# Optimization experiments

Hardware: AMD Instinct MI355X
Metric: run time of the kernel (lower is better)

The kernel has to match this reference:

```python
import jax, jax.numpy as jnp
import numpy as np
from jax import lax

B, IN_N, OUT_N, SEQ, HID = 8, 16, 16, 256, 64
NUM_C = 64 + 3  # grid_size + spline_order
EPS_LN = 1e-5


def setup_inputs():
    key = jax.random.key(0)
    k = jax.random.split(key, 8)
    f32 = jnp.float32
    return {
        "x_in": jax.random.normal(k[0], (B, IN_N, SEQ, HID), f32),
        "proj_x_prev": jax.random.normal(k[1], (B, IN_N, SEQ, HID), f32),
        "spline_weights": jax.random.normal(k[2], (IN_N, OUT_N, NUM_C), f32) * 0.1,
        "base_scales": 0.6 + 0.1 * jax.random.normal(k[3], (IN_N, OUT_N), f32),
        "tau": jax.random.normal(k[4], (IN_N, OUT_N), f32) * 0.1 + 0.1,
        "temperature": jnp.array(1.0, f32),
        "omiga": jnp.full((IN_N, OUT_N), 0.2, f32),
        "W2": jax.random.normal(k[5], (OUT_N, HID, HID), f32) / np.sqrt(HID).astype(np.float32),
        "b_param": jnp.zeros((OUT_N, SEQ, HID), f32),
        "ln_w": jnp.ones((OUT_N, HID), f32),
        "ln_b": jnp.zeros((OUT_N, HID), f32),
        "alpha": jnp.full((OUT_N,), 0.5, f32),
        "beta": jnp.ones((OUT_N,), f32),
        "gamma": jnp.full((OUT_N,), 0.5, f32),
        "theta": jnp.ones((OUT_N,), f32),
        "conv_w": jax.random.normal(k[6], (OUT_N, HID, 1, 3, 3), f32) * 0.1,
    }


def _layernorm(x, w=None, b=None):
    mu = jnp.mean(x, -1, keepdims=True)
    var = jnp.mean((x - mu) ** 2, -1, keepdims=True)
    y = (x - mu) / jnp.sqrt(var + EPS_LN)
    if w is not None:
        y = y * w + b
    return y


def _dwconv(x, w):
    # x: [b, C, 16, 16]; w: [C, 1, 3, 3]; depthwise conv, SAME padding
    return lax.conv_general_dilated(
        x, w, (1, 1), "SAME",
        dimension_numbers=("NCHW", "OIHW", "NCHW"),
        feature_group_count=x.shape[1])


def _forward(x_in, proj_x_prev, spline_weights, base_scales, tau, temperature,
             omiga, W2, b_param, ln_w, ln_b, alpha, beta, gamma, theta, conv_w):
    b, in_n, seq, feat = x_in.shape
    num_c = spline_weights.shape[-1]
    grid = jnp.linspace(-1.0, 1.0, num_c)
    h = 2.0 / (num_c - 1)

    x_energy = jnp.mean(x_in, -1)  # [b,i,s]
    x_norm = jnp.clip(
        x_energy / (jnp.max(jnp.abs(x_energy), -1, keepdims=True) + 1e-8),
        -0.99, 0.99)

    # cubic B-spline basis (masked branches -> nested where)
    dist = jnp.abs(x_norm[..., None] - grid) / h  # [b,i,s,c]
    basis = jnp.where(dist < 1.0, 2.0 / 3.0 - dist ** 2 + dist ** 3 / 2.0,
            jnp.where(dist < 2.0, (2.0 - dist) ** 3 / 6.0, jnp.zeros_like(dist)))

    base_feat = jax.nn.silu(x_norm)[:, :, None, :] * base_scales[None, :, :, None]  # [b,i,j,s]
    spline_feat = jnp.einsum("bisc,ijc->bijs", basis, spline_weights)
    edge_resp = base_feat + spline_feat
    # [b,i,j,s,f]
    activated = (edge_resp[..., None] + jnp.abs(omiga)[None, :, :, None, None]) * x_in[:, :, None]

    t_val = jnp.abs(temperature) + 1e-4
    edge_energies = jnp.mean(jnp.abs(activated), axis=(-1, -2))  # [b,i,j]
    tau_abs = jnp.abs(tau)  # [i,j]
    mask = jax.nn.sigmoid((edge_energies - tau_abs[None]) / t_val)  # [b,i,j]

    # attention kernel W1, vectorized over output neuron j
    mid = in_n // 2
    mult = edge_energies / (tau_abs[None] + 1e-8)  # [b,i,j]
    wp = proj_x_prev[:, :, None] * (mult * mask)[..., None, None]  # [b,i,j,s,d]
    d = wp.shape[-1]
    K = jnp.transpose(wp[:, :mid], (0, 2, 3, 1, 4)).reshape(b, -1, seq, mid * d)
    Q = jnp.transpose(wp[:, mid:2 * mid], (0, 2, 3, 1, 4)).reshape(b, -1, seq, mid * d)
    K, Q = _layernorm(K), _layernorm(Q)
    raw = jnp.einsum("bjsk,bjtk->bjst", K, Q) / (jnp.sqrt(jnp.float32(mid * d)) * t_val)
    W1 = jax.nn.softmax(raw, axis=-1)  # [b,j,s,s]

    # masked mean over input neurons -> per-neuron SplineWeightLayer (vectorized)
    x = jnp.mean(activated * mask[..., None, None], axis=1)  # [b,j,s,f]
    xn = _layernorm(x, ln_w[None, :, None, :], ln_b[None, :, None, :])
    x_prime = jnp.einsum("bjsf,jfo->bjso", xn, W2) + b_param[None]  # [b,j,s,o]
    o = x_prime.shape[-1]

    # depthwise 3x3 conv on 16x16 spatial view, per-j kernels
    xsp = jnp.transpose(x_prime, (1, 0, 3, 2)).reshape(-1, b, o, 16, 16)  # [j,b,o,16,16]
    w3 = jax.vmap(_dwconv)(xsp, conv_w)  # [j,b,o,16,16]
    w3 = jnp.transpose(w3.reshape(-1, b, o, seq), (1, 0, 3, 2))  # [b,j,s,o]

    eye = jnp.eye(seq, dtype=x_prime.dtype)
    ak = (jnp.abs(beta)[None, :, None, None] * W1
          + jnp.abs(alpha)[None, :, None, None] * eye[None, None])
    glob = jnp.einsum("bjst,bjto->bjso", ak, x_prime)
    combined = glob + jnp.abs(theta)[None, :, None, None] * w3
    # residual_proj is Identity since in_hidden == out_hidden
    out = combined + gamma[None, :, None, None] * x
    return out, x_prime  # both [b, out_n, seq, out_hidden]


def reference(x_in, proj_x_prev, spline_weights, base_scales, tau, temperature,
              omiga, W2, b_param, ln_w, ln_b, alpha, beta, gamma, theta, conv_w):
    return _forward(x_in, proj_x_prev, spline_weights, base_scales, tau, temperature,
                    omiga, W2, b_param, ln_w, ln_b, alpha, beta, gamma, theta, conv_w)
```

## Files before the change

kernel.cpp:

```cpp
#include <hip/hip_runtime.h>

#define EPSLN 1e-5f

typedef short bf16x8 __attribute__((ext_vector_type(8)));
typedef float f32x4 __attribute__((ext_vector_type(4)));
typedef unsigned short u16;
typedef unsigned short u16x8 __attribute__((ext_vector_type(8)));

__device__ __forceinline__ float wsum(float v){
  #pragma unroll
  for(int o=32;o;o>>=1) v += __shfl_xor(v,o);
  return v;
}
__device__ __forceinline__ float wmax(float v){
  #pragma unroll
  for(int o=32;o;o>>=1) v = fmaxf(v,__shfl_xor(v,o));
  return v;
}
__device__ __forceinline__ u16 f2bf(float f){
  unsigned int u = __float_as_uint(f);
  u = (u + 0x7FFFu + ((u>>16)&1u)) >> 16;
  return (u16)u;
}
__device__ __forceinline__ float bf2f(u16 h){
  return __uint_as_float(((unsigned int)h)<<16);
}

__global__ void __launch_bounds__(256) kA(
                   const float* __restrict__ xin, const float* __restrict__ p,
                   const float* __restrict__ W2,
                   float* __restrict__ xe, float* __restrict__ xa,
                   float* __restrict__ Sv, float* __restrict__ SSv,
                   u16* __restrict__ xinb, u16* __restrict__ phi, u16* __restrict__ plo,
                   u16* __restrict__ w2B){
  int t = threadIdx.x;
  int rl = t>>3, q = t&7;
  int row = blockIdx.x*32 + rl;
  const float4* xr = (const float4*)(xin + row*64 + q*8);
  const float4* pr = (const float4*)(p   + row*64 + q*8);
  float s1=0.f,s2=0.f,s3=0.f,s4=0.f;
  u16x8 xb, ph, pl;
  #pragma unroll
  for(int k=0;k<2;k++){
    float4 xv = xr[k];
    float4 pv = pr[k];
    s1 += xv.x+xv.y+xv.z+xv.w;
    s2 += fabsf(xv.x)+fabsf(xv.y)+fabsf(xv.z)+fabsf(xv.w);
    s3 += pv.x+pv.y+pv.z+pv.w;
    s4 += pv.x*pv.x+pv.y*pv.y+pv.z*pv.z+pv.w*pv.w;
    int o = k*4;
    xb[o+0]=f2bf(xv.x); xb[o+1]=f2bf(xv.y); xb[o+2]=f2bf(xv.z); xb[o+3]=f2bf(xv.w);
    u16 h0=f2bf(pv.x), h1=f2bf(pv.y), h2=f2bf(pv.z), h3=f2bf(pv.w);
    ph[o+0]=h0; ph[o+1]=h1; ph[o+2]=h2; ph[o+3]=h3;
    pl[o+0]=f2bf(pv.x-bf2f(h0)); pl[o+1]=f2bf(pv.y-bf2f(h1));
    pl[o+2]=f2bf(pv.z-bf2f(h2)); pl[o+3]=f2bf(pv.w-bf2f(h3));
  }
  *(u16x8*)(xinb + row*64 + q*8) = xb;
  *(u16x8*)(phi  + row*64 + q*8) = ph;
  *(u16x8*)(plo  + row*64 + q*8) = pl;
  s1 += __shfl_xor(s1,1); s1 += __shfl_xor(s1,2); s1 += __shfl_xor(s1,4);
  s2 += __shfl_xor(s2,1); s2 += __shfl_xor(s2,2); s2 += __shfl_xor(s2,4);
  s3 += __shfl_xor(s3,1); s3 += __shfl_xor(s3,2); s3 += __shfl_xor(s3,4);
  s4 += __shfl_xor(s4,1); s4 += __shfl_xor(s4,2); s4 += __shfl_xor(s4,4);
  if(q==0){ xe[row]=s1*(1.f/64.f); xa[row]=s2*(1.f/64.f); Sv[row]=s3; SSv[row]=s4; }
  if(blockIdx.x<16){
    int j = blockIdx.x;
    for(int idx=threadIdx.x; idx<4096; idx+=256){
      int f = idx>>6, o = idx&63;
      float v = W2[j*4096 + idx];
      int ks = f>>5, kb = (f>>3)&3, i = f&7;
      int nt = o>>4, col = o&15;
      int ln = kb*16 + col;
      w2B[((j*2+ks)*4 + nt)*512 + ln*8 + i] = f2bf(v);
    }
  }
}

__global__ void __launch_bounds__(256) kBE(
                   const float* __restrict__ xe, const float* __restrict__ sw,
                   const float* __restrict__ bs, const float* __restrict__ om,
                   const float* __restrict__ xa, const float* __restrict__ tau,
                   const float* __restrict__ temp,
                   u16* __restrict__ er2b, float* __restrict__ mask,
                   float* __restrict__ cc,
                   const u16* __restrict__ phi, const u16* __restrict__ plo,
                   float* __restrict__ G){
  __shared__ __align__(16) unsigned char shm[32768];
  int tid = threadIdx.x;
  if(blockIdx.x < 128){
    float* swL = (float*)shm;
    float* bsL = swL + 1072;
    float* omL = bsL + 16;
    float* red = omL + 16;
    float* redE= red + 4;
    int bi = blockIdx.x;
    int i = bi & 15;
    int w = tid>>6, lane = tid&63;
    for(int k=tid;k<16*67;k+=256) swL[k] = sw[i*16*67 + k];
    if(tid<16){ bsL[tid]=bs[i*16+tid]; omL[tid]=fabsf(om[i*16+tid]); }
    float v = xe[bi*256+tid];
    float m = wmax(fabsf(v));
    if(lane==0) red[w]=m;
    __syncthreads();
    m = fmaxf(fmaxf(red[0],red[1]),fmaxf(red[2],red[3]));
    float xn = v/(m+1e-8f);
    xn = fminf(fmaxf(xn,-0.99f),0.99f);
    float sil = xn/(1.f+expf(-xn));
    float vv = (xn+1.f)*33.f;
    int c0 = (int)floorf(vv)-1;
    float acc[16];
    #pragma unroll
    for(int j=0;j<16;j++) acc[j]=0.f;
    #pragma unroll
    for(int k=0;k<4;k++){
      int c = c0+k;
      if(c<0||c>66) continue;
      float d = fabsf(vv-(float)c);
      float bas = d<1.f ? (2.f/3.f - d*d + d*d*d*0.5f)
                : (d<2.f ? (2.f-d)*(2.f-d)*(2.f-d)*(1.f/6.f) : 0.f);
      #pragma unroll
      for(int j=0;j<16;j++) acc[j] += bas*swL[j*67+c];
    }
    float xav = xa[bi*256+tid];
    #pragma unroll
    for(int j=0;j<16;j++){
      float ev = sil*bsL[j] + acc[j] + omL[j];
      er2b[(bi*16+j)*256+tid] = f2bf(ev);
      float pe = wsum(fabsf(ev)*xav);
      if(lane==0) redE[j*4+w]=pe;
    }
    __syncthreads();
    if(tid<16){
      float e = (redE[tid*4+0]+redE[tid*4+1]+redE[tid*4+2]+redE[tid*4+3])*(1.f/256.f);
      float tv = fabsf(temp[0])+1e-4f;
      float ta = fabsf(tau[i*16+tid]);
      float mk = 1.f/(1.f+expf(-(e-ta)/tv));
      mask[bi*16+tid]=mk;
      cc[bi*16+tid]= e/(ta+1e-8f)*mk;
    }
  } else {
    u16* AfB = (u16*)shm;
    u16* BfB = AfB + 8192;
    int e = blockIdx.x - 128;
    int b = e&7, m = (e>>3)&7, sx = (e>>6)&3, ty = e>>8;
    int bm = b*8+m;
    int s0 = sx*64, t0 = ty*64;
    int row = tid>>2, dseg = tid&3;
    size_t offA = ((size_t)(b*16+m  )*256 + s0 + row)*64 + dseg*16;
    size_t offB = ((size_t)(b*16+m+8)*256 + t0 + row)*64 + dseg*16;
    int d0 = dseg*16;
    int ks0 = d0>>5, kb0 = (d0>>3)&3;
    int ks1 = (d0+8)>>5, kb1 = ((d0+8)>>3)&3;
    int lr = row&15, stile = row>>4;
    #define AOFF(h,stl,ks,ln) (((((h)*4+(stl))*2+(ks))*64 + (ln))*8)
    {
      uint4 v0 = *(const uint4*)(phi + offA);
      uint4 v1 = *(const uint4*)(phi + offA + 8);
      *(uint4*)(AfB + AOFF(0,stile,ks0,kb0*16+lr)) = v0;
      *(uint4*)(AfB + AOFF(0,stile,ks1,kb1*16+lr)) = v1;
      uint4 w0 = *(const uint4*)(plo + offA);
      uint4 w1 = *(const uint4*)(plo + offA + 8);
      *(uint4*)(AfB + AOFF(1,stile,ks0,kb0*16+lr)) = w0;
      *(uint4*)(AfB + AOFF(1,stile,ks1,kb1*16+lr)) = w1;
      uint4 x0 = *(const uint4*)(phi + offB);
      uint4 x1 = *(const uint4*)(phi + offB + 8);
      *(uint4*)(BfB + AOFF(0,stile,ks0,kb0*16+lr)) = x0;
      *(uint4*)(BfB + AOFF(0,stile,ks1,kb1*16+lr)) = x1;
      uint4 y0 = *(const uint4*)(plo + offB);
      uint4 y1 = *(const uint4*)(plo + offB + 8);
      *(uint4*)(BfB + AOFF(1,stile,ks0,kb0*16+lr)) = y0;
      *(uint4*)(BfB + AOFF(1,stile,ks1,kb1*16+lr)) = y1;
    }
    __syncthreads();
    int w = tid>>6, lane = tid&63;
    bf16x8 ah0 = *(const bf16x8*)(AfB + AOFF(0,w,0,lane));
    bf16x8 ah1 = *(const bf16x8*)(AfB + AOFF(0,w,1,lane));
    bf16x8 al0 = *(const bf16x8*)(AfB + AOFF(1,w,0,lane));
    bf16x8 al1 = *(const bf16x8*)(AfB + AOFF(1,w,1,lane));
    f32x4 acc[4];
    #pragma unroll
    for(int tt=0;tt<4;tt++) acc[tt] = (f32x4){0.f,0.f,0.f,0.f};
    #pragma unroll
    for(int tt=0;tt<4;tt++){
      bf16x8 bh0 = *(const bf16x8*)(BfB + AOFF(0,tt,0,lane));
      bf16x8 bh1 = *(const bf16x8*)(BfB + AOFF(0,tt,1,lane));
      bf16x8 bl0 = *(const bf16x8*)(BfB + AOFF(1,tt,0,lane));
      bf16x8 bl1 = *(const bf16x8*)(BfB + AOFF(1,tt,1,lane));
      acc[tt] = __builtin_amdgcn_mfma_f32_16x16x32_bf16(ah0, bh0, acc[tt], 0,0,0);
      acc[tt] = __builtin_amdgcn_mfma_f32_16x16x32_bf16(ah1, bh1, acc[tt], 0,0,0);
      acc[tt] = __builtin_amdgcn_mfma_f32_16x16x32_bf16(ah0, bl0, acc[tt], 0,0,0);
      acc[tt] = __builtin_amdgcn_mfma_f32_16x16x32_bf16(ah1, bl1, acc[tt], 0,0,0);
      acc[tt] = __builtin_amdgcn_mfma_f32_16x16x32_bf16(al0, bh0, acc[tt], 0,0,0);
      acc[tt] = __builtin_amdgcn_mfma_f32_16x16x32_bf16(al1, bh1, acc[tt], 0,0,0);
    }
    int col = lane&15, r4 = lane>>4;
    #pragma unroll
    for(int tt=0;tt<4;tt++){
      #pragma unroll
      for(int r=0;r<4;r++){
        G[((size_t)bm*256 + s0 + w*16 + r4*4 + r)*256 + t0 + tt*16 + col] = acc[tt][r];
      }
    }
    #undef AOFF
  }
}

__global__ void __launch_bounds__(256) kD(
                   const u16* __restrict__ xinb, const u16* __restrict__ er2b,
                   const float* __restrict__ mask, const u16* __restrict__ w2B,
                   const float* __restrict__ lnw, const float* __restrict__ lnb,
                   const float* __restrict__ bp,
                   u16* __restrict__ xoutb, float* __restrict__ xp,
                   u16* __restrict__ xpB){
  int b = blockIdx.x, j = blockIdx.y, st = blockIdx.z;
  int tid = threadIdx.x, w = tid>>6, lane = tid&63;
  __shared__ __align__(16) u16 xnS[16*64];
  __shared__ float mcL[16];
  if(tid<16) mcL[tid]=mask[(b*16+tid)*16+j];
  __syncthreads();
  int bj = b*16+j;
  unsigned char* xnB = (unsigned char*)xnS;
  int ss = lane>>4, fq = lane&15;
  int sl = w*4 + ss;
  int s  = st*16 + sl;
  float4 lw4 = *(const float4*)(lnw + j*64 + fq*4);
  float4 lb4 = *(const float4*)(lnb + j*64 + fq*4);
  float acc0=0.f,acc1=0.f,acc2=0.f,acc3=0.f;
  #pragma unroll
  for(int i=0;i<16;i++){
    float er = bf2f(er2b[((b*16+i)*16+j)*256+s])*mcL[i];
    ushort4 xv = *(const ushort4*)(xinb + ((size_t)(b*16+i)*256+s)*64 + fq*4);
    acc0 += er*bf2f(xv.x);
    acc1 += er*bf2f(xv.y);
    acc2 += er*bf2f(xv.z);
    acc3 += er*bf2f(xv.w);
  }
  acc0*=(1.f/16.f); acc1*=(1.f/16.f); acc2*=(1.f/16.f); acc3*=(1.f/16.f);
  {
    u16 pk[4]={f2bf(acc0),f2bf(acc1),f2bf(acc2),f2bf(acc3)};
    *(ushort4*)(xoutb + ((size_t)bj*256+s)*64 + fq*4) = *(ushort4*)pk;
  }
  float part = acc0+acc1+acc2+acc3;
  part += __shfl_xor(part,1); part += __shfl_xor(part,2);
  part += __shfl_xor(part,4); part += __shfl_xor(part,8);
  float mu = part*(1.f/64.f);
  float d0=acc0-mu, d1=acc1-mu, d2=acc2-mu, d3=acc3-mu;
  float p2 = d0*d0+d1*d1+d2*d2+d3*d3;
  p2 += __shfl_xor(p2,1); p2 += __shfl_xor(p2,2);
  p2 += __shfl_xor(p2,4); p2 += __shfl_xor(p2,8);
  float rstd = rsqrtf(p2*(1.f/64.f)+EPSLN);
  {
    u16 xn[4] = { f2bf(d0*rstd*lw4.x + lb4.x), f2bf(d1*rstd*lw4.y + lb4.y),
                  f2bf(d2*rstd*lw4.z + lb4.z), f2bf(d3*rstd*lw4.w + lb4.w) };
    *(ushort4*)(xnB + ((sl*128 + fq*8) ^ ((sl&7)<<4))) = *(ushort4*)xn;
  }
  __syncthreads();
  f32x4 acc = {0.f,0.f,0.f,0.f};
  int m = lane&15, kb = lane>>4;
  #pragma unroll
  for(int ks=0;ks<2;ks++){
    bf16x8 a = *(const bf16x8*)(xnB + ((m*128 + ks*64 + kb*16) ^ ((m&7)<<4)));
    bf16x8 bfr = *(const bf16x8*)(w2B + ((j*2+ks)*4 + w)*512 + lane*8);
    acc = __builtin_amdgcn_mfma_f32_16x16x32_bf16(a, bfr, acc, 0, 0, 0);
  }
  int f = w*16 + m;
  u16 pk[4];
  #pragma unroll
  for(int r=0;r<4;r++){
    int si = kb*4 + r;
    int s2 = st*16 + si;
    float xpr = acc[r] + bp[((size_t)j*256+s2)*64+f];
    xp[((size_t)bj*256+s2)*64+f] = xpr;
    pk[r] = f2bf(xpr);
  }
  int s0 = st*16 + kb*4;
  int flat = ((s0>>5)*4 + w)*512 + ((s0>>3)&3)*128 + m*8 + (s0&7);
  *(ushort4*)(xpB + (size_t)bj*16384 + flat) = *(ushort4*)pk;
}

__global__ void __launch_bounds__(256) kF(
    const float* __restrict__ G, const float* __restrict__ cc,
    const float* __restrict__ Sv, const float* __restrict__ SSv,
    const float* __restrict__ xp, const u16* __restrict__ xpB,
    const float* __restrict__ cw,
    const u16* __restrict__ xarrb, const float* __restrict__ temp,
    const float* __restrict__ alpha, const float* __restrict__ beta,
    const float* __restrict__ gamma_, const float* __restrict__ theta,
    float* __restrict__ out){
  int b = blockIdx.x, jp = blockIdx.y, st = blockIdx.z;
  int j0 = jp*4;
  int tid = threadIdx.x, w = tid>>6, lane = tid&63;
  __shared__ __align__(16) unsigned char ovl[26112];
  unsigned char* prA = ovl;
  unsigned char* prB = ovl + 8192;
  float* mQL = (float*)(ovl + 16384);
  float* rQL = (float*)(ovl + 20480);
  float* mKL = (float*)(ovl + 24576);
  float* rKL = (float*)(ovl + 24832);
  float* xpT = (float*)ovl;
  float tv = fabsf(temp[0])+1e-4f;
  float inv = 1.f/(sqrtf(512.f)*tv);
  float aM0[8],aM1[8],aM2[8],aM3[8];
  {
    int t = tid;
    float sk0=0,sk1=0,sk2=0,sk3=0, ssk0=0,ssk1=0,ssk2=0,ssk3=0;
    float sq0=0,sq1=0,sq2=0,sq3=0, ssq0=0,ssq1=0,ssq2=0,ssq3=0;
    #pragma unroll
    for(int m=0;m<8;m++){
      float4 ck = *(const float4*)(cc + (b*16+m  )*16 + j0);
      float4 cq = *(const float4*)(cc + (b*16+m+8)*16 + j0);
      aM0[m]=ck.x*cq.x; aM1[m]=ck.y*cq.y; aM2[m]=ck.z*cq.z; aM3[m]=ck.w*cq.w;
      float svk = Sv [(b*16+m)*256+t];
      float ssvk= SSv[(b*16+m)*256+t];
      float svq = Sv [(b*16+m+8)*256+t];
      float ssvq= SSv[(b*16+m+8)*256+t];
      sk0 += ck.x*svk; ssk0 += ck.x*ck.x*ssvk;
      sk1 += ck.y*svk; ssk1 += ck.y*ck.y*ssvk;
      sk2 += ck.z*svk; ssk2 += ck.z*ck.z*ssvk;
      sk3 += ck.w*svk; ssk3 += ck.w*ck.w*ssvk;
      sq0 += cq.x*svq; ssq0 += cq.x*cq.x*ssvq;
      sq1 += cq.y*svq; ssq1 += cq.y*cq.y*ssvq;
      sq2 += cq.z*svq; ssq2 += cq.z*cq.z*ssvq;
      sq3 += cq.w*svq; ssq3 += cq.w*cq.w*ssvq;
    }
    float mq;
    mq = sq0*(1.f/512.f); mQL[0*256+t]=mq; rQL[0*256+t]=rsqrtf(ssq0*(1.f/512.f)-mq*mq+EPSLN);
    mq = sq1*(1.f/512.f); mQL[1*256+t]=mq; rQL[1*256+t]=rsqrtf(ssq1*(1.f/512.f)-mq*mq+EPSLN);
    mq = sq2*(1.f/512.f); mQL[2*256+t]=mq; rQL[2*256+t]=rsqrtf(ssq2*(1.f/512.f)-mq*mq+EPSLN);
    mq = sq3*(1.f/512.f); mQL[3*256+t]=mq; rQL[3*256+t]=rsqrtf(ssq3*(1.f/512.f)-mq*mq+EPSLN);
    if((t>>4)==st){
      int si = t&15;
      float mk;
      mk = sk0*(1.f/512.f); mKL[0*16+si]=mk; rKL[0*16+si]=rsqrtf(ssk0*(1.f/512.f)-mk*mk+EPSLN);
      mk = sk1*(1.f/512.f); mKL[1*16+si]=mk; rKL[1*16+si]=rsqrtf(ssk1*(1.f/512.f)-mk*mk+EPSLN);
      mk = sk2*(1.f/512.f); mKL[2*16+si]=mk; rKL[2*16+si]=rsqrtf(ssk2*(1.f/512.f)-mk*mk+EPSLN);
      mk = sk3*(1.f/512.f); mKL[3*16+si]=mk; rKL[3*16+si]=rsqrtf(ssk3*(1.f/512.f)-mk*mk+EPSLN);
    }
  }
  __syncthreads();
  const float* Gb = G + (size_t)(b*8)*65536;
  float4 mQ4a = *(const float4*)&mQL[0*256+lane*4];
  float4 rQ4a = *(const float4*)&rQL[0*256+lane*4];
  float4 mQ4b = *(const float4*)&mQL[1*256+lane*4];
  float4 rQ4b = *(const float4*)&rQL[1*256+lane*4];
  float4 mQ4c = *(const float4*)&mQL[2*256+lane*4];
  float4 rQ4c = *(const float4*)&rQL[2*256+lane*4];
  float4 mQ4d = *(const float4*)&mQL[3*256+lane*4];
  float4 rQ4d = *(const float4*)&rQL[3*256+lane*4];
  ushort4 pk2[4], pk3[4];
  #pragma unroll
  for(int q=0;q<4;q++){
    int si = w*4+q;
    int s = st*16 + si;
    f32x4 dt0={0.f,0.f,0.f,0.f}, dt1={0.f,0.f,0.f,0.f};
    f32x4 dt2={0.f,0.f,0.f,0.f}, dt3={0.f,0.f,0.f,0.f};
    #pragma unroll
    for(int m=0;m<8;m++){
      f32x4 g4 = *(const f32x4*)(Gb + (size_t)m*65536 + s*256 + lane*4);
      dt0 += aM0[m]*g4; dt1 += aM1[m]*g4;
      dt2 += aM2[m]*g4; dt3 += aM3[m]*g4;
    }
    #define SMK(JJ, DT, MQ, RQ, PKOUT) { \
      float mKs = 512.f*mKL[JJ*16+si], rKs = rKL[JJ*16+si]; \
      float e0 = __expf((DT[0] - mKs*MQ.x)*rKs*RQ.x*inv); \
      float e1 = __expf((DT[1] - mKs*MQ.y)*rKs*RQ.y*inv); \
      float e2 = __expf((DT[2] - mKs*MQ.z)*rKs*RQ.z*inv); \
      float e3 = __expf((DT[3] - mKs*MQ.w)*rKs*RQ.w*inv); \
      float isf = 1.f/wsum(e0+e1+e2+e3); \
      u16 pk[4] = {f2bf(e0*isf), f2bf(e1*isf), f2bf(e2*isf), f2bf(e3*isf)}; \
      PKOUT = *(ushort4*)pk; }
    ushort4 t0v, t1v;
    SMK(0, dt0, mQ4a, rQ4a, t0v)
    SMK(1, dt1, mQ4b, rQ4b, t1v)
    int poff = (si*512 + lane*8) ^ ((si&7)<<4);
    *(ushort4*)(prA + poff) = t0v;
    *(ushort4*)(prB + poff) = t1v;
    SMK(2, dt2, mQ4c, rQ4c, pk2[q])
    SMK(3, dt3, mQ4d, rQ4d, pk3[q])
    #undef SMK
  }
  __syncthreads();
  int m_ = lane&15, kb = lane>>4;
  f32x4 av0={0.f,0.f,0.f,0.f}, av1={0.f,0.f,0.f,0.f};
  f32x4 av2={0.f,0.f,0.f,0.f}, av3={0.f,0.f,0.f,0.f};
  const u16* xpB0 = xpB + (size_t)(b*16+j0  )*16384;
  const u16* xpB1 = xpB + (size_t)(b*16+j0+1)*16384;
  const u16* xpB2 = xpB + (size_t)(b*16+j0+2)*16384;
  const u16* xpB3 = xpB + (size_t)(b*16+j0+3)*16384;
  #pragma unroll
  for(int ks=0;ks<8;ks++){
    int aoff = (m_*512 + ks*64 + kb*16) ^ ((m_&7)<<4);
    int boff = ((ks*4 + w)*64 + lane)*8;
    bf16x8 a0 = *(const bf16x8*)(prA + aoff);
    bf16x8 a1 = *(const bf16x8*)(prB + aoff);
    av0 = __builtin_amdgcn_mfma_f32_16x16x32_bf16(a0, *(const bf16x8*)(xpB0 + boff), av0, 0,0,0);
    av1 = __builtin_amdgcn_mfma_f32_16x16x32_bf16(a1, *(const bf16x8*)(xpB1 + boff), av1, 0,0,0);
  }
  __syncthreads();
  #pragma unroll
  for(int q=0;q<4;q++){
    int si = w*4+q;
    int poff = (si*512 + lane*8) ^ ((si&7)<<4);
    *(ushort4*)(prA + poff) = pk2[q];
    *(ushort4*)(prB + poff) = pk3[q];
  }
  __syncthreads();
  #pragma unroll
  for(int ks=0;ks<8;ks++){
    int aoff = (m_*512 + ks*64 + kb*16) ^ ((m_&7)<<4);
    int boff = ((ks*4 + w)*64 + lane)*8;
    bf16x8 a2 = *(const bf16x8*)(prA + aoff);
    bf16x8 a3 = *(const bf16x8*)(prB + aoff);
    av2 = __builtin_amdgcn_mfma_f32_16x16x32_bf16(a2, *(const bf16x8*)(xpB2 + boff), av2, 0,0,0);
    av3 = __builtin_amdgcn_mfma_f32_16x16x32_bf16(a3, *(const bf16x8*)(xpB3 + boff), av3, 0,0,0);
  }
  int f = w*16 + m_;
  #pragma unroll
  for(int pass=0; pass<2; pass++){
    __syncthreads();
    for(int idx4 = tid; idx4 < 1536; idx4 += 256){
      int jj = idx4 / 768;
      int rem = idx4 - jj*768;
      int rr_i = rem >> 8;
      int pos = rem & 255;
      int ci = pos>>4, f4 = pos&15;
      int grow = st - 1 + rr_i;
      float4 v = {0.f,0.f,0.f,0.f};
      if(grow>=0 && grow<16){
        v = *(const float4*)(xp + ((size_t)(b*16+j0+pass*2+jj)*256 + grow*16 + ci)*64 + f4*4);
      }
      *(float4*)(xpT + ((jj*3+rr_i)*16+ci)*68 + f4*4) = v;
    }
    __syncthreads();
    #pragma unroll
    for(int jj=0;jj<2;jj++){
      int j = j0 + pass*2 + jj;
      int bj = b*16+j;
      f32x4 acc = pass==0 ? (jj?av1:av0) : (jj?av3:av2);
      float al = fabsf(alpha[j]), be=fabsf(beta[j]), th=fabsf(theta[j]), ga=gamma_[j];
      const float* wq = cw + (j*64+f)*9;
      float w0=wq[0],w1=wq[1],w2=wq[2],w3v=wq[3],w4=wq[4],w5=wq[5],w6=wq[6],w7=wq[7],w8=wq[8];
      #pragma unroll
      for(int r=0;r<4;r++){
        int si = kb*4 + r;
        int s = st*16 + si;
        float gl = acc[r];
        float cv=0.f;
        #pragma unroll
        for(int dr=0;dr<3;dr++){
          float kw0 = dr==0?w0:(dr==1?w3v:w6);
          float kw1 = dr==0?w1:(dr==1?w4:w7);
          float kw2 = dr==0?w2:(dr==1?w5:w8);
          const float* rowp = xpT + ((jj*3+dr)*16)*68;
          if(si>0)  cv += rowp[(si-1)*68+f]*kw0;
                    cv += rowp[(si  )*68+f]*kw1;
          if(si<15) cv += rowp[(si+1)*68+f]*kw2;
        }
        float diag = xpT[((jj*3+1)*16+si)*68+f];
        size_t gi = ((size_t)bj*256+s)*64+f;
        out[gi] = be*gl + al*diag + th*cv + ga*bf2f(xarrb[gi]);
      }
    }
  }
}

extern "C" void kernel_launch(void* const* d_in, const int* in_sizes, int n_in,
                              void* d_out, int out_size, void* d_ws, size_t ws_size,
                              hipStream_t stream) {
  const float* xin = (const float*)d_in[0];
  const float* pxp = (const float*)d_in[1];
  const float* sw  = (const float*)d_in[2];
  const float* bs  = (const float*)d_in[3];
  const float* tau = (const float*)d_in[4];
  const float* temp= (const float*)d_in[5];
  const float* om  = (const float*)d_in[6];
  const float* W2  = (const float*)d_in[7];
  const float* bp  = (const float*)d_in[8];
  const float* lnw = (const float*)d_in[9];
  const float* lnb = (const float*)d_in[10];
  const float* alpha=(const float*)d_in[11];
  const float* beta= (const float*)d_in[12];
  const float* gam = (const float*)d_in[13];
  const float* theta=(const float*)d_in[14];
  const float* cw  = (const float*)d_in[15];
  float* outp = (float*)d_out;
  float* xpo  = outp + 2097152;

  float* ws  = (float*)d_ws;
  float* xe  = ws;
  float* xa  = xe + 32768;
  float* Sv  = xa + 32768;
  float* SSv = Sv + 32768;
  u16*   er2b= (u16*)(SSv + 32768);
  float* mask= (float*)(er2b) + 524288;
  float* ccv = mask + 2048;
  float* Gv  = ccv + 2048;
  u16* xvb = (u16*)(Gv + 4194304);
  u16* xpB = xvb + 2097152;
  u16* w2B = xpB + 2097152;
  u16* xinb= w2B + 65536;
  u16* phi = xinb + 2097152;
  u16* plo = phi + 2097152;

  kA<<<1024,256,0,stream>>>(xin,pxp,W2,xe,xa,Sv,SSv,xinb,phi,plo,w2B);
  kBE<<<1152,256,0,stream>>>(xe,sw,bs,om,xa,tau,temp,er2b,mask,ccv,phi,plo,Gv);
  kD<<<dim3(8,16,16),256,0,stream>>>(xinb,er2b,mask,w2B,lnw,lnb,bp,xvb,xpo,xpB);
  kF<<<dim3(8,4,16),256,0,stream>>>(Gv,ccv,Sv,SSv,xpo,xpB,cw,xvb,temp,
                                    alpha,beta,gam,theta,outp);
}
```

Baseline: 55.26 us.

## Precompute Q/K layernorm stats once in extra kD blocks instead of per kF block

The per-(b,j) mean and rsqrt-variance statistics for Q and K were recomputed redundantly in every kF block, which is 16 seq tiles times 4 j values, followed by a block barrier. They are now computed once by 128 extra blocks appended to the kD grid, written to workspace, and read directly by kF from global memory. This removes redundant Sv/SSv reads, arithmetic and a __syncthreads from kF. In exchange it adds global round-trips and shifts the workspace layout, placing Gv after four new buffers.

```diff
diff --git a/kernel.cpp b/kernel.cpp
--- a/kernel.cpp
+++ b/kernel.cpp
@@ -211,9 +211,38 @@
                    const float* __restrict__ lnw, const float* __restrict__ lnb,
                    const float* __restrict__ bp,
                    u16* __restrict__ xoutb, float* __restrict__ xp,
-                   u16* __restrict__ xpB){
-  int b = blockIdx.x, j = blockIdx.y, st = blockIdx.z;
-  int tid = threadIdx.x, w = tid>>6, lane = tid&63;
+                   u16* __restrict__ xpB,
+                   const float* __restrict__ Sv, const float* __restrict__ SSv,
+                   const float* __restrict__ cc,
+                   float* __restrict__ mKv, float* __restrict__ rKv,
+                   float* __restrict__ mQv, float* __restrict__ rQv){
+  int bid = blockIdx.x;
+  int tid = threadIdx.x;
+  if(bid >= 2048){
+    int sid = bid - 2048;
+    int b = sid&7, j = sid>>3;
+    int t = tid;
+    float sk=0,ssk=0,sq=0,ssq=0;
+    #pragma unroll
+    for(int m=0;m<8;m++){
+      float ck = cc[(b*16+m)*16+j];
+      float cq = cc[(b*16+m+8)*16+j];
+      sk  += ck*Sv[(b*16+m)*256+t];
+      ssk += ck*ck*SSv[(b*16+m)*256+t];
+      sq  += cq*Sv[(b*16+m+8)*256+t];
+      ssq += cq*cq*SSv[(b*16+m+8)*256+t];
+    }
+    float mk = sk*(1.f/512.f);
+    float vk = ssk*(1.f/512.f) - mk*mk;
+    float mq = sq*(1.f/512.f);
+    float vq = ssq*(1.f/512.f) - mq*mq;
+    int o = (b*16+j)*256+t;
+    mKv[o]=mk; rKv[o]=rsqrtf(vk+EPSLN);
+    mQv[o]=mq; rQv[o]=rsqrtf(vq+EPSLN);
+    return;
+  }
+  int b = bid&7, j = (bid>>3)&15, st = bid>>7;
+  int w = tid>>6, lane = tid&63;
   __shared__ __align__(16) u16 xnS[16*64];
   __shared__ float mcL[16];
   if(tid<16) mcL[tid]=mask[(b*16+tid)*16+j];
@@ -280,7 +309,8 @@
 
 __global__ void __launch_bounds__(256) kF(
     const float* __restrict__ G, const float* __restrict__ cc,
-    const float* __restrict__ Sv, const float* __restrict__ SSv,
+    const float* __restrict__ mKv, const float* __restrict__ rKv,
+    const float* __restrict__ mQv, const float* __restrict__ rQv,
     const float* __restrict__ xp, const u16* __restrict__ xpB,
     const float* __restrict__ cw,
     const u16* __restrict__ xarrb, const float* __restrict__ temp,
@@ -293,60 +323,26 @@
   __shared__ __align__(16) unsigned char ovl[26112];
   unsigned char* prA = ovl;
   unsigned char* prB = ovl + 8192;
-  float* mQL = (float*)(ovl + 16384);
-  float* rQL = (float*)(ovl + 20480);
-  float* mKL = (float*)(ovl + 24576);
-  float* rKL = (float*)(ovl + 24832);
   float* xpT = (float*)ovl;
   float tv = fabsf(temp[0])+1e-4f;
   float inv = 1.f/(sqrtf(512.f)*tv);
   float aM0[8],aM1[8],aM2[8],aM3[8];
-  {
-    int t = tid;
-    float sk0=0,sk1=0,sk2=0,sk3=0, ssk0=0,ssk1=0,ssk2=0,ssk3=0;
-    float sq0=0,sq1=0,sq2=0,sq3=0, ssq0=0,ssq1=0,ssq2=0,ssq3=0;
-    #pragma unroll
-    for(int m=0;m<8;m++){
-      float4 ck = *(const float4*)(cc + (b*16+m  )*16 + j0);
-      float4 cq = *(const float4*)(cc + (b*16+m+8)*16 + j0);
-      aM0[m]=ck.x*cq.x; aM1[m]=ck.y*cq.y; aM2[m]=ck.z*cq.z; aM3[m]=ck.w*cq.w;
-      float svk = Sv [(b*16+m)*256+t];
-      float ssvk= SSv[(b*16+m)*256+t];
-      float svq = Sv [(b*16+m+8)*256+t];
-      float ssvq= SSv[(b*16+m+8)*256+t];
-      sk0 += ck.x*svk; ssk0 += ck.x*ck.x*ssvk;
-      sk1 += ck.y*svk; ssk1 += ck.y*ck.y*ssvk;
-      sk2 += ck.z*svk; ssk2 += ck.z*ck.z*ssvk;
-      sk3 += ck.w*svk; ssk3 += ck.w*ck.w*ssvk;
-      sq0 += cq.x*svq; ssq0 += cq.x*cq.x*ssvq;
-      sq1 += cq.y*svq; ssq1 += cq.y*cq.y*ssvq;
-      sq2 += cq.z*svq; ssq2 += cq.z*cq.z*ssvq;
-      sq3 += cq.w*svq; ssq3 += cq.w*cq.w*ssvq;
-    }
-    float mq;
-    mq = sq0*(1.f/512.f); mQL[0*256+t]=mq; rQL[0*256+t]=rsqrtf(ssq0*(1.f/512.f)-mq*mq+EPSLN);
-    mq = sq1*(1.f/512.f); mQL[1*256+t]=mq; rQL[1*256+t]=rsqrtf(ssq1*(1.f/512.f)-mq*mq+EPSLN);
-    mq = sq2*(1.f/512.f); mQL[2*256+t]=mq; rQL[2*256+t]=rsqrtf(ssq2*(1.f/512.f)-mq*mq+EPSLN);
-    mq = sq3*(1.f/512.f); mQL[3*256+t]=mq; rQL[3*256+t]=rsqrtf(ssq3*(1.f/512.f)-mq*mq+EPSLN);
-    if((t>>4)==st){
-      int si = t&15;
-      float mk;
-      mk = sk0*(1.f/512.f); mKL[0*16+si]=mk; rKL[0*16+si]=rsqrtf(ssk0*(1.f/512.f)-mk*mk+EPSLN);
-      mk = sk1*(1.f/512.f); mKL[1*16+si]=mk; rKL[1*16+si]=rsqrtf(ssk1*(1.f/512.f)-mk*mk+EPSLN);
-      mk = sk2*(1.f/512.f); mKL[2*16+si]=mk; rKL[2*16+si]=rsqrtf(ssk2*(1.f/512.f)-mk*mk+EPSLN);
-      mk = sk3*(1.f/512.f); mKL[3*16+si]=mk; rKL[3*16+si]=rsqrtf(ssk3*(1.f/512.f)-mk*mk+EPSLN);
-    }
-  }
-  __syncthreads();
+  #pragma unroll
+  for(int m=0;m<8;m++){
+    float4 ck = *(const float4*)(cc + (b*16+m  )*16 + j0);
+    float4 cq = *(const float4*)(cc + (b*16+m+8)*16 + j0);
+    aM0[m]=ck.x*cq.x; aM1[m]=ck.y*cq.y; aM2[m]=ck.z*cq.z; aM3[m]=ck.w*cq.w;
+  }
+  int bj0 = b*16+j0;
+  float4 mQ4a = *(const float4*)(mQv + (size_t)(bj0  )*256 + lane*4);
+  float4 rQ4a = *(const float4*)(rQv + (size_t)(bj0  )*256 + lane*4);
+  float4 mQ4b = *(const float4*)(mQv + (size_t)(bj0+1)*256 + lane*4);
+  float4 rQ4b = *(const float4*)(rQv + (size_t)(bj0+1)*256 + lane*4);
+  float4 mQ4c = *(const float4*)(mQv + (size_t)(bj0+2)*256 + lane*4);
+  float4 rQ4c = *(const float4*)(rQv + (size_t)(bj0+2)*256 + lane*4);
+  float4 mQ4d = *(const float4*)(mQv + (size_t)(bj0+3)*256 + lane*4);
+  float4 rQ4d = *(const float4*)(rQv + (size_t)(bj0+3)*256 + lane*4);
   const float* Gb = G + (size_t)(b*8)*65536;
-  float4 mQ4a = *(const float4*)&mQL[0*256+lane*4];
-  float4 rQ4a = *(const float4*)&rQL[0*256+lane*4];
-  float4 mQ4b = *(const float4*)&mQL[1*256+lane*4];
-  float4 rQ4b = *(const float4*)&rQL[1*256+lane*4];
-  float4 mQ4c = *(const float4*)&mQL[2*256+lane*4];
-  float4 rQ4c = *(const float4*)&rQL[2*256+lane*4];
-  float4 mQ4d = *(const float4*)&mQL[3*256+lane*4];
-  float4 rQ4d = *(const float4*)&rQL[3*256+lane*4];
   ushort4 pk2[4], pk3[4];
   #pragma unroll
   for(int q=0;q<4;q++){
@@ -361,7 +357,7 @@
       dt2 += aM2[m]*g4; dt3 += aM3[m]*g4;
     }
     #define SMK(JJ, DT, MQ, RQ, PKOUT) { \
-      float mKs = 512.f*mKL[JJ*16+si], rKs = rKL[JJ*16+si]; \
+      float mKs = 512.f*mKv[(size_t)(bj0+JJ)*256 + s], rKs = rKv[(size_t)(bj0+JJ)*256 + s]; \
       float e0 = __expf((DT[0] - mKs*MQ.x)*rKs*RQ.x*inv); \
       float e1 = __expf((DT[1] - mKs*MQ.y)*rKs*RQ.y*inv); \
       float e2 = __expf((DT[2] - mKs*MQ.z)*rKs*RQ.z*inv); \
@@ -383,10 +379,10 @@
   int m_ = lane&15, kb = lane>>4;
   f32x4 av0={0.f,0.f,0.f,0.f}, av1={0.f,0.f,0.f,0.f};
   f32x4 av2={0.f,0.f,0.f,0.f}, av3={0.f,0.f,0.f,0.f};
-  const u16* xpB0 = xpB + (size_t)(b*16+j0  )*16384;
-  const u16* xpB1 = xpB + (size_t)(b*16+j0+1)*16384;
-  const u16* xpB2 = xpB + (size_t)(b*16+j0+2)*16384;
-  const u16* xpB3 = xpB + (size_t)(b*16+j0+3)*16384;
+  const u16* xpB0 = xpB + (size_t)(bj0  )*16384;
+  const u16* xpB1 = xpB + (size_t)(bj0+1)*16384;
+  const u16* xpB2 = xpB + (size_t)(bj0+2)*16384;
+  const u16* xpB3 = xpB + (size_t)(bj0+3)*16384;
   #pragma unroll
   for(int ks=0;ks<8;ks++){
     int aoff = (m_*512 + ks*64 + kb*16) ^ ((m_&7)<<4);
@@ -494,7 +490,11 @@
   u16*   er2b= (u16*)(SSv + 32768);
   float* mask= (float*)(er2b) + 524288;
   float* ccv = mask + 2048;
-  float* Gv  = ccv + 2048;
+  float* mKv = ccv + 2048;
+  float* rKv = mKv + 32768;
+  float* mQv = rKv + 32768;
+  float* rQv = mQv + 32768;
+  float* Gv  = rQv + 32768;
   u16* xvb = (u16*)(Gv + 4194304);
   u16* xpB = xvb + 2097152;
   u16* w2B = xpB + 2097152;
@@ -504,7 +504,8 @@
 
   kA<<<1024,256,0,stream>>>(xin,pxp,W2,xe,xa,Sv,SSv,xinb,phi,plo,w2B);
   kBE<<<1152,256,0,stream>>>(xe,sw,bs,om,xa,tau,temp,er2b,mask,ccv,phi,plo,Gv);
-  kD<<<dim3(8,16,16),256,0,stream>>>(xinb,er2b,mask,w2B,lnw,lnb,bp,xvb,xpo,xpB);
-  kF<<<dim3(8,4,16),256,0,stream>>>(Gv,ccv,Sv,SSv,xpo,xpB,cw,xvb,temp,
+  kD<<<2176,256,0,stream>>>(xinb,er2b,mask,w2B,lnw,lnb,bp,xvb,xpo,xpB,
+                            Sv,SSv,ccv,mKv,rKv,mQv,rQv);
+  kF<<<dim3(8,4,16),256,0,stream>>>(Gv,ccv,mKv,rKv,mQv,rQv,xpo,xpB,cw,xvb,temp,
                                     alpha,beta,gam,theta,outp);
 }
```

New measurement: 54.61 us. Within noise of the previous version (-1.2%).
